# Kernel optimization log

Hardware: AMD Instinct MI355X
Metric: run time of the kernel (lower is better)

## Reference

```python
import jax, jax.numpy as jnp
import numpy as np

DIM = 768
H = 12
HD = DIM // H  # 64
B = 16
N = 1025  # cls token + 1024 patches; RoPE applied to tokens 1:


def setup_inputs() -> dict:
    key = jax.random.key(0)
    k1, k2, k3, k4, k5, k6 = jax.random.split(key, 6)
    x = jax.random.normal(k1, (B, N, DIM), dtype=jnp.float32)
    # rotary angles for the N-1 non-cls tokens, HD//2 freq pairs
    theta = jax.random.uniform(k2, (N - 1, HD // 2), dtype=jnp.float32) * 2.0 * jnp.pi
    freqs_cos = jnp.cos(theta)
    freqs_sin = jnp.sin(theta)
    W_qkv = jax.random.normal(k3, (3 * DIM, DIM), dtype=jnp.float32) * 0.02
    W_proj = jax.random.normal(k4, (DIM, DIM), dtype=jnp.float32) * 0.02
    b_proj = jax.random.normal(k5, (DIM,), dtype=jnp.float32) * 0.02
    return {"x": x, "freqs_cos": freqs_cos, "freqs_sin": freqs_sin,
            "W_qkv": W_qkv, "W_proj": W_proj, "b_proj": b_proj}


def _apply_rope(t, cos, sin):
    # t: [b, h, m, d]; cos/sin: [m, d/2]. Pairs are interleaved (even, odd),
    # matching torch.view_as_complex on a (..., d/2, 2) reshape.
    tr = t[..., 0::2]
    ti = t[..., 1::2]
    cos = cos[None, None, :, :]
    sin = sin[None, None, :, :]
    out_r = tr * cos - ti * sin
    out_i = tr * sin + ti * cos
    # interleave back: (..., d/2, 2) -> (..., d)
    out = jnp.stack([out_r, out_i], axis=-1)
    return out.reshape(t.shape)


def reference(x, freqs_cos, freqs_sin, W_qkv, W_proj, b_proj):
    b, n, dim = x.shape
    h, hd = H, HD
    scale = hd ** -0.5

    qkv = jnp.einsum('bnd,ed->bne', x, W_qkv)            # [b, n, 3*dim]
    qkv = qkv.reshape(b, n, 3, h, hd)
    q = jnp.transpose(qkv[:, :, 0], (0, 2, 1, 3))         # [b, h, n, hd]
    k = jnp.transpose(qkv[:, :, 1], (0, 2, 1, 3))
    v = jnp.transpose(qkv[:, :, 2], (0, 2, 1, 3))

    # RoPE on all tokens except the cls token (index 0)
    q = jnp.concatenate([q[:, :, :1], _apply_rope(q[:, :, 1:], freqs_cos, freqs_sin)], axis=2)
    k = jnp.concatenate([k[:, :, :1], _apply_rope(k[:, :, 1:], freqs_cos, freqs_sin)], axis=2)

    dots = jnp.einsum('bhid,bhjd->bhij', q, k) * scale    # [b, h, n, n]
    attn = jax.nn.softmax(dots, axis=-1)
    out = jnp.einsum('bhij,bhjd->bhid', attn, v)          # [b, h, n, hd]
    out = jnp.transpose(out, (0, 2, 1, 3)).reshape(b, n, dim)
    out = jnp.einsum('bnd,ed->bne', out, W_proj) + b_proj
    return out
```

## Files before the change

### kernel.cpp

```cpp
#include <hip/hip_runtime.h>
#include <stdint.h>

#define NH 12
#define HD64 64
#define SEQ 1025
#define M_ROWS (16 * SEQ)
#define DIM 768
#define NPAD 1088

typedef __attribute__((ext_vector_type(8))) short bf16x8;
typedef __attribute__((ext_vector_type(4))) float f32x4;
typedef __attribute__((ext_vector_type(4))) short s16x4;

#define VMCNT(n) asm volatile("s_waitcnt vmcnt(" #n ")" ::: "memory")
#define LGKMCNT0 asm volatile("s_waitcnt lgkmcnt(0)" ::: "memory")

__device__ __forceinline__ short f2bf_rne(float f) {
    union { float f; uint32_t u; } c; c.f = f;
    uint32_t u = c.u + 0x7fffu + ((c.u >> 16) & 1u);
    return (short)(u >> 16);
}

__device__ __forceinline__ int cvt_pk_bf16(float lo, float hi) {
    int r;
    asm("v_cvt_pk_bf16_f32 %0, %1, %2" : "=v"(r) : "v"(lo), "v"(hi));
    return r;
}

__device__ __forceinline__ void gload_lds16(const void* g, void* l) {
    __builtin_amdgcn_global_load_lds(
        (const __attribute__((address_space(1))) void*)g,
        (__attribute__((address_space(3))) void*)l, 16, 0, 0);
}

__device__ __forceinline__ int xcd_chunk_swizzle(int orig, int nwg) {
    int q = nwg >> 3, r = nwg & 7;
    int xcd = orig & 7, i = orig >> 3;
    int start = (xcd < r) ? xcd * (q + 1) : r * (q + 1) + (xcd - r) * q;
    return start + i;
}

__global__ void f2bf_kernel(const float* __restrict__ in, short* __restrict__ out, int n4) {
    int i = blockIdx.x * blockDim.x + threadIdx.x;
    if (i < n4) {
        f32x4 f = ((const f32x4*)in)[i];
        s16x4 o;
        o[0] = f2bf_rne(f[0]); o[1] = f2bf_rne(f[1]);
        o[2] = f2bf_rne(f[2]); o[3] = f2bf_rne(f[3]);
        ((s16x4*)out)[i] = o;
    }
}

__global__ __launch_bounds__(256) void qkv_gemm_kernel(
    const short* __restrict__ xb, const short* __restrict__ wb,
    const float* __restrict__ fcos, const float* __restrict__ fsin,
    short* __restrict__ Qb, short* __restrict__ Kb, short* __restrict__ VTb)
{
    __shared__ short Alds[3][128 * 32];
    __shared__ short Blds[3][128 * 32];
    const int tid = threadIdx.x;
    const int lane = tid & 63, w = tid >> 6;
    const int wm = w >> 1, wn = w & 1;
    const int lr = lane & 15, lg = lane >> 4;
    const int tile = xcd_chunk_swizzle(blockIdx.x, 129 * 18);
    const int mt = tile / 18, nt = tile - (tile / 18) * 18;

    const int c0 = tid, c1 = 256 + tid;
    int ra0 = mt * 128 + (c0 >> 2); if (ra0 > M_ROWS - 1) ra0 = M_ROWS - 1;
    int ra1 = mt * 128 + (c1 >> 2); if (ra1 > M_ROWS - 1) ra1 = M_ROWS - 1;
    const short* gA0 = xb + (size_t)ra0 * DIM + (c0 & 3) * 8;
    const short* gA1 = xb + (size_t)ra1 * DIM + (c1 & 3) * 8;
    const short* gB0 = wb + (size_t)(nt * 128 + (c0 >> 2)) * DIM + (c0 & 3) * 8;
    const short* gB1 = wb + (size_t)(nt * 128 + (c1 >> 2)) * DIM + (c1 & 3) * 8;
    short* lA0 = &Alds[0][0] + c0 * 8;
    short* lA1 = &Alds[0][0] + c1 * 8;
    short* lB0 = &Blds[0][0] + c0 * 8;
    short* lB1 = &Blds[0][0] + c1 * 8;

    auto stage = [&](int buf, int kt) {
        const int ko = kt * 32;
        const int lo = buf * (128 * 32);
        gload_lds16(gA0 + ko, lA0 + lo);
        gload_lds16(gA1 + ko, lA1 + lo);
        gload_lds16(gB0 + ko, lB0 + lo);
        gload_lds16(gB1 + ko, lB1 + lo);
    };

    f32x4 acc[4][4];
#pragma unroll
    for (int i = 0; i < 4; i++)
#pragma unroll
        for (int j = 0; j < 4; j++) acc[i][j] = (f32x4)0.0f;

    stage(0, 0); stage(1, 1); stage(2, 2);

    int cur = 0;
    for (int t = 0; t < 24; ++t) {
        if (t <= 21) { VMCNT(8); } else if (t == 22) { VMCNT(4); } else { VMCNT(0); }
        __builtin_amdgcn_s_barrier();

        bf16x8 af[4], bfr[4];
        const short* Ab = &Alds[0][0] + cur * (128 * 32);
        const short* Bb = &Blds[0][0] + cur * (128 * 32);
#pragma unroll
        for (int mi = 0; mi < 4; mi++)
            af[mi] = *(const bf16x8*)&Ab[(wm * 64 + mi * 16 + lr) * 32 + lg * 8];
#pragma unroll
        for (int ni = 0; ni < 4; ni++)
            bfr[ni] = *(const bf16x8*)&Bb[(wn * 64 + ni * 16 + lr) * 32 + lg * 8];

        if (t <= 20) {
            LGKMCNT0;
            __builtin_amdgcn_s_barrier();
            stage(cur, t + 3);
        }

#pragma unroll
        for (int mi = 0; mi < 4; mi++)
#pragma unroll
            for (int ni = 0; ni < 4; ni++)
                acc[mi][ni] = __builtin_amdgcn_mfma_f32_16x16x32_bf16(af[mi], bfr[ni], acc[mi][ni], 0, 0, 0);

        cur = (cur == 2) ? 0 : cur + 1;
    }

#pragma unroll
    for (int mi = 0; mi < 4; mi++) {
        int mbase = mt * 128 + wm * 64 + mi * 16 + lg * 4;
#pragma unroll
        for (int j = 0; j < 4; j++) {
            int m = mbase + j;
            bool valid = (m < M_ROWS);
            int mm = valid ? m : 0;
            int b = mm / SEQ;
            int n = mm - b * SEQ;
#pragma unroll
            for (int ni = 0; ni < 4; ni++) {
                int e = nt * 128 + wn * 64 + ni * 16 + lr;
                int qkv = e / DIM;
                int rem = e - qkv * DIM;
                int h = rem >> 6, d = rem & 63;
                float v = acc[mi][ni][j];
                float vo = __shfl_xor(v, 1);
                float outv = v;
                if (qkv < 2 && n > 0) {
                    float cs = fcos[(n - 1) * 32 + (d >> 1)];
                    float sn = fsin[(n - 1) * 32 + (d >> 1)];
                    outv = (d & 1) ? (vo * sn + v * cs) : (v * cs - vo * sn);
                }
                if (qkv == 0) outv *= 0.180336881f;
                if (valid) {
                    short bv = f2bf_rne(outv);
                    size_t bh = (size_t)b * NH + h;
                    if (qkv == 0)      Qb[(bh * SEQ + n) * HD64 + d] = bv;
                    else if (qkv == 1) Kb[(bh * SEQ + n) * HD64 + d] = bv;
                    else               VTb[(bh * HD64 + d) * NPAD + n] = bv;
                }
            }
        }
    }
}

__global__ __launch_bounds__(256) void attn_kernel(
    const short* __restrict__ Qb, const short* __restrict__ Kb,
    const short* __restrict__ VTb, short* __restrict__ AO)
{
    __shared__ short Klds[2][64 * 64];
    __shared__ short Vlds[2][64 * 64];
    __shared__ int Plds[4][16 * 32];
    const int tid = threadIdx.x;
    const int lane = tid & 63, w = tid >> 6;
    const int lr = lane & 15, lg = lane >> 4;
    const int tile = xcd_chunk_swizzle(blockIdx.x, 17 * 192);
    const int bh = tile / 17, qt = tile - (tile / 17) * 17;
    const int b = bh / NH, h = bh - b * NH;

    const short* Qp = Qb + (size_t)bh * SEQ * HD64;
    const short* Kp = Kb + (size_t)bh * SEQ * HD64;
    const short* Vp = VTb + (size_t)bh * HD64 * NPAD;

    int qr = qt * 64 + w * 16 + lr; if (qr > SEQ - 1) qr = SEQ - 1;
    bf16x8 qf0 = *(const bf16x8*)&Qp[(size_t)qr * HD64 + 0 + lg * 8];
    bf16x8 qf1 = *(const bf16x8*)&Qp[(size_t)qr * HD64 + 32 + lg * 8];

    float m_i = -1e30f, l_i = 0.f;
    f32x4 acc[4];
#pragma unroll
    for (int vt = 0; vt < 4; vt++) acc[vt] = (f32x4)0.0f;

    int* pw = &Plds[w][0];
    const int pswz = (lr & 3) << 3;

    auto stageKV = [&](int buf, int t) {
        int k0 = t * 64;
#pragma unroll
        for (int i = 0; i < 2; i++) {
            int c = i * 256 + tid;
            int row = c >> 3, ccd = c & 7;
            int cl = ccd ^ (row & 7);
            int krow = k0 + row; if (krow > SEQ - 1) krow = SEQ - 1;
            gload_lds16(Kp + (size_t)krow * HD64 + cl * 8, &Klds[buf][c * 8]);
            gload_lds16(Vp + (size_t)row * NPAD + k0 + cl * 8, &Vlds[buf][c * 8]);
        }
    };

    stageKV(0, 0);
    asm volatile("s_waitcnt vmcnt(0)" ::: "memory");
    __syncthreads();

    for (int t = 0; t < 17; ++t) {
        int cur = t & 1;
        if (t < 16) stageKV(cur ^ 1, t + 1);

        f32x4 s[4];
#pragma unroll
        for (int k16 = 0; k16 < 4; k16++) {
            int krow = k16 * 16 + lr;
            bf16x8 kf0 = *(const bf16x8*)&Klds[cur][krow * 64 + ((0 + lg) ^ (krow & 7)) * 8];
            bf16x8 kf1 = *(const bf16x8*)&Klds[cur][krow * 64 + ((4 + lg) ^ (krow & 7)) * 8];
            f32x4 d = (f32x4)0.0f;
            d = __builtin_amdgcn_mfma_f32_16x16x32_bf16(kf0, qf0, d, 0, 0, 0);
            d = __builtin_amdgcn_mfma_f32_16x16x32_bf16(kf1, qf1, d, 0, 0, 0);
            s[k16] = d;
        }
        if (t == 16) {
            s[0][0] = (lg == 0) ? s[0][0] : -1e30f;
            s[0][1] = -1e30f; s[0][2] = -1e30f; s[0][3] = -1e30f;
#pragma unroll
            for (int k16 = 1; k16 < 4; k16++) { s[k16][0] = -1e30f; s[k16][1] = -1e30f; s[k16][2] = -1e30f; s[k16][3] = -1e30f; }
        }

        float a0 = fmaxf(s[0][0], s[0][1]), a1 = fmaxf(s[0][2], s[0][3]);
        float a2 = fmaxf(s[1][0], s[1][1]), a3 = fmaxf(s[1][2], s[1][3]);
        float a4 = fmaxf(s[2][0], s[2][1]), a5 = fmaxf(s[2][2], s[2][3]);
        float a6 = fmaxf(s[3][0], s[3][1]), a7 = fmaxf(s[3][2], s[3][3]);
        float b0 = fmaxf(fmaxf(a0, a1), fmaxf(a2, a3));
        float b1 = fmaxf(fmaxf(a4, a5), fmaxf(a6, a7));
        float pmax = fmaxf(b0, b1);
        pmax = fmaxf(pmax, __shfl_xor(pmax, 16));
        pmax = fmaxf(pmax, __shfl_xor(pmax, 32));

        if (__any(pmax > m_i + 11.54f)) {
            float mnew = fmaxf(m_i, pmax);
            float sc = exp2f(m_i - mnew);
            m_i = mnew;
            l_i *= sc;
#pragma unroll
            for (int j = 0; j < 4; j++) {
                float scj = __shfl(sc, 4 * lg + j);
#pragma unroll
                for (int vt = 0; vt < 4; vt++) acc[vt][j] *= scj;
            }
        }

#pragma unroll
        for (int k16 = 0; k16 < 4; k16++) {
#pragma unroll
            for (int j = 0; j < 4; j++) s[k16][j] = exp2f(s[k16][j] - m_i);
        }
        float r0 = (s[0][0] + s[0][1]) + (s[0][2] + s[0][3]);
        float r1 = (s[1][0] + s[1][1]) + (s[1][2] + s[1][3]);
        float r2 = (s[2][0] + s[2][1]) + (s[2][2] + s[2][3]);
        float r3 = (s[3][0] + s[3][1]) + (s[3][2] + s[3][3]);
        float rowsum = (r0 + r1) + (r2 + r3);
        rowsum += __shfl_xor(rowsum, 16);
        rowsum += __shfl_xor(rowsum, 32);
        l_i += rowsum;

#pragma unroll
        for (int k16 = 0; k16 < 4; k16++) {
            int pk0 = cvt_pk_bf16(s[k16][0], s[k16][1]);
            int pk1 = cvt_pk_bf16(s[k16][2], s[k16][3]);
            int pbase = 8 * k16 + 2 * lg;
            pw[lr * 32 + ((pbase + 0) ^ pswz)] = pk0;
            pw[lr * 32 + ((pbase + 1) ^ pswz)] = pk1;
        }
        bf16x8 pa0 = *(const bf16x8*)&pw[lr * 32 + ((4 * lg) ^ pswz)];
        bf16x8 pa1 = *(const bf16x8*)&pw[lr * 32 + ((16 + 4 * lg) ^ pswz)];

#pragma unroll
        for (int vt = 0; vt < 4; vt++) {
            int dr = vt * 16 + lr;
            bf16x8 vf0 = *(const bf16x8*)&Vlds[cur][dr * 64 + ((0 + lg) ^ (dr & 7)) * 8];
            bf16x8 vf1 = *(const bf16x8*)&Vlds[cur][dr * 64 + ((4 + lg) ^ (dr & 7)) * 8];
            acc[vt] = __builtin_amdgcn_mfma_f32_16x16x32_bf16(pa0, vf0, acc[vt], 0, 0, 0);
            acc[vt] = __builtin_amdgcn_mfma_f32_16x16x32_bf16(pa1, vf1, acc[vt], 0, 0, 0);
        }

        asm volatile("s_waitcnt vmcnt(0)" ::: "memory");
        __syncthreads();
    }

    float inv[4];
#pragma unroll
    for (int j = 0; j < 4; j++) inv[j] = 1.0f / __shfl(l_i, 4 * lg + j);
#pragma unroll
    for (int vt = 0; vt < 4; vt++) {
#pragma unroll
        for (int j = 0; j < 4; j++) {
            int qrow = qt * 64 + w * 16 + lg * 4 + j;
            if (qrow < SEQ) {
                AO[((size_t)(b * SEQ + qrow)) * DIM + h * HD64 + vt * 16 + lr] =
                    f2bf_rne(acc[vt][j] * inv[j]);
            }
        }
    }
}

__global__ __launch_bounds__(256) void proj_gemm_kernel(
    const short* __restrict__ ab, const short* __restrict__ wb,
    const float* __restrict__ bias, float* __restrict__ out)
{
    __shared__ short Alds[3][128 * 32];
    __shared__ short Blds[3][128 * 32];
    const int tid = threadIdx.x;
    const int lane = tid & 63, w = tid >> 6;
    const int wm = w >> 1, wn = w & 1;
    const int lr = lane & 15, lg = lane >> 4;
    const int tile = xcd_chunk_swizzle(blockIdx.x, 129 * 6);
    const int mt = tile / 6, nt = tile - (tile / 6) * 6;

    const int c0 = tid, c1 = 256 + tid;
    int ra0 = mt * 128 + (c0 >> 2); if (ra0 > M_ROWS - 1) ra0 = M_ROWS - 1;
    int ra1 = mt * 128 + (c1 >> 2); if (ra1 > M_ROWS - 1) ra1 = M_ROWS - 1;
    const short* gA0 = ab + (size_t)ra0 * DIM + (c0 & 3) * 8;
    const short* gA1 = ab + (size_t)ra1 * DIM + (c1 & 3) * 8;
    const short* gB0 = wb + (size_t)(nt * 128 + (c0 >> 2)) * DIM + (c0 & 3) * 8;
    const short* gB1 = wb + (size_t)(nt * 128 + (c1 >> 2)) * DIM + (c1 & 3) * 8;
    short* lA0 = &Alds[0][0] + c0 * 8;
    short* lA1 = &Alds[0][0] + c1 * 8;
    short* lB0 = &Blds[0][0] + c0 * 8;
    short* lB1 = &Blds[0][0] + c1 * 8;

    auto stage = [&](int buf, int kt) {
        const int ko = kt * 32;
        const int lo = buf * (128 * 32);
        gload_lds16(gA0 + ko, lA0 + lo);
        gload_lds16(gA1 + ko, lA1 + lo);
        gload_lds16(gB0 + ko, lB0 + lo);
        gload_lds16(gB1 + ko, lB1 + lo);
    };

    f32x4 acc[4][4];
#pragma unroll
    for (int i = 0; i < 4; i++)
#pragma unroll
        for (int j = 0; j < 4; j++) acc[i][j] = (f32x4)0.0f;

    stage(0, 0); stage(1, 1); stage(2, 2);

    int cur = 0;
    for (int t = 0; t < 24; ++t) {
        if (t <= 21) { VMCNT(8); } else if (t == 22) { VMCNT(4); } else { VMCNT(0); }
        __builtin_amdgcn_s_barrier();

        bf16x8 af[4], bfr[4];
        const short* Ab = &Alds[0][0] + cur * (128 * 32);
        const short* Bb = &Blds[0][0] + cur * (128 * 32);
#pragma unroll
        for (int mi = 0; mi < 4; mi++)
            af[mi] = *(const bf16x8*)&Ab[(wm * 64 + mi * 16 + lr) * 32 + lg * 8];
#pragma unroll
        for (int ni = 0; ni < 4; ni++)
            bfr[ni] = *(const bf16x8*)&Bb[(wn * 64 + ni * 16 + lr) * 32 + lg * 8];

        if (t <= 20) {
            LGKMCNT0;
            __builtin_amdgcn_s_barrier();
            stage(cur, t + 3);
        }

#pragma unroll
        for (int mi = 0; mi < 4; mi++)
#pragma unroll
            for (int ni = 0; ni < 4; ni++)
                acc[mi][ni] = __builtin_amdgcn_mfma_f32_16x16x32_bf16(af[mi], bfr[ni], acc[mi][ni], 0, 0, 0);

        cur = (cur == 2) ? 0 : cur + 1;
    }

#pragma unroll
    for (int ni = 0; ni < 4; ni++) {
        int e = nt * 128 + wn * 64 + ni * 16 + lr;
        float bv = bias[e];
#pragma unroll
        for (int mi = 0; mi < 4; mi++) {
#pragma unroll
            for (int j = 0; j < 4; j++) {
                int m = mt * 128 + wm * 64 + mi * 16 + lg * 4 + j;
                if (m < M_ROWS) out[(size_t)m * DIM + e] = acc[mi][ni][j] + bv;
            }
        }
    }
}

extern "C" void kernel_launch(void* const* d_in, const int* in_sizes, int n_in,
                              void* d_out, int out_size, void* d_ws, size_t ws_size,
                              hipStream_t stream) {
    const float* x     = (const float*)d_in[0];
    const float* fcos  = (const float*)d_in[1];
    const float* fsin  = (const float*)d_in[2];
    const float* wqkv  = (const float*)d_in[3];
    const float* wproj = (const float*)d_in[4];
    const float* bproj = (const float*)d_in[5];
    float* out = (float*)d_out;

    char* ws = (char*)d_ws;
    size_t off = 0;
    auto salloc = [&](size_t bytes) { void* p = ws + off; off += (bytes + 255) & ~(size_t)255; return p; };
    short* xb     = (short*)salloc((size_t)M_ROWS * DIM * 2);
    short* wqkvb  = (short*)salloc((size_t)2304 * DIM * 2);
    short* wprojb = (short*)salloc((size_t)DIM * DIM * 2);
    short* Qb     = (short*)salloc((size_t)192 * SEQ * HD64 * 2);
    short* Kb     = (short*)salloc((size_t)192 * SEQ * HD64 * 2);
    short* VTb    = (short*)salloc((size_t)192 * HD64 * NPAD * 2);
    short* AO     = (short*)salloc((size_t)M_ROWS * DIM * 2);

    {
        int n4 = M_ROWS * DIM / 4;
        f2bf_kernel<<<(n4 + 255) / 256, 256, 0, stream>>>(x, xb, n4);
    }
    {
        int n4 = 2304 * DIM / 4;
        f2bf_kernel<<<(n4 + 255) / 256, 256, 0, stream>>>(wqkv, wqkvb, n4);
    }
    {
        int n4 = DIM * DIM / 4;
        f2bf_kernel<<<(n4 + 255) / 256, 256, 0, stream>>>(wproj, wprojb, n4);
    }

    qkv_gemm_kernel<<<129 * 18, 256, 0, stream>>>(xb, wqkvb, fcos, fsin, Qb, Kb, VTb);
    attn_kernel<<<17 * 192, 256, 0, stream>>>(Qb, Kb, VTb, AO);
    proj_gemm_kernel<<<129 * 6, 256, 0, stream>>>(AO, wprojb, bproj, out);
}
```

Baseline: 336.4 us.

## Widen QKV GEMM tile, swizzle LDS, fuse casts, add MFMA priority hints

The QKV GEMM N-tile is widened from 128 to 256, so each wave computes 4x8 MFMA tiles and the grid halves. Its A/B LDS layout gets an XOR swizzle to reduce bank conflicts on fragment reads. The three fp32-to-bf16 cast launches are merged into one kernel, and s_setprio hints are wrapped around the MFMA blocks in attention. The wider tile raises register and LDS use per block (launch_bounds 256,2), which may limit occupancy.

```diff
diff --git a/kernel.cpp b/kernel.cpp
--- a/kernel.cpp
+++ b/kernel.cpp
@@ -40,74 +40,88 @@
     return start + i;
 }
 
-__global__ void f2bf_kernel(const float* __restrict__ in, short* __restrict__ out, int n4) {
+__global__ void f2bf3_kernel(const float* __restrict__ a, short* __restrict__ ao, int na4,
+                             const float* __restrict__ b, short* __restrict__ bo, int nb4,
+                             const float* __restrict__ c, short* __restrict__ co, int nc4) {
     int i = blockIdx.x * blockDim.x + threadIdx.x;
-    if (i < n4) {
-        f32x4 f = ((const f32x4*)in)[i];
-        s16x4 o;
-        o[0] = f2bf_rne(f[0]); o[1] = f2bf_rne(f[1]);
-        o[2] = f2bf_rne(f[2]); o[3] = f2bf_rne(f[3]);
-        ((s16x4*)out)[i] = o;
-    }
-}
-
-__global__ __launch_bounds__(256) void qkv_gemm_kernel(
+    const float* src; short* dst; int idx;
+    if (i < na4) { src = a; dst = ao; idx = i; }
+    else if (i < na4 + nb4) { src = b; dst = bo; idx = i - na4; }
+    else if (i < na4 + nb4 + nc4) { src = c; dst = co; idx = i - na4 - nb4; }
+    else return;
+    f32x4 f = ((const f32x4*)src)[idx];
+    s16x4 o;
+    o[0] = f2bf_rne(f[0]); o[1] = f2bf_rne(f[1]);
+    o[2] = f2bf_rne(f[2]); o[3] = f2bf_rne(f[3]);
+    ((s16x4*)dst)[idx] = o;
+}
+
+__global__ __launch_bounds__(256, 2) void qkv_gemm_kernel(
     const short* __restrict__ xb, const short* __restrict__ wb,
     const float* __restrict__ fcos, const float* __restrict__ fsin,
     short* __restrict__ Qb, short* __restrict__ Kb, short* __restrict__ VTb)
 {
     __shared__ short Alds[3][128 * 32];
-    __shared__ short Blds[3][128 * 32];
+    __shared__ short Blds[3][256 * 32];
     const int tid = threadIdx.x;
     const int lane = tid & 63, w = tid >> 6;
     const int wm = w >> 1, wn = w & 1;
     const int lr = lane & 15, lg = lane >> 4;
-    const int tile = xcd_chunk_swizzle(blockIdx.x, 129 * 18);
-    const int mt = tile / 18, nt = tile - (tile / 18) * 18;
-
-    const int c0 = tid, c1 = 256 + tid;
-    int ra0 = mt * 128 + (c0 >> 2); if (ra0 > M_ROWS - 1) ra0 = M_ROWS - 1;
-    int ra1 = mt * 128 + (c1 >> 2); if (ra1 > M_ROWS - 1) ra1 = M_ROWS - 1;
-    const short* gA0 = xb + (size_t)ra0 * DIM + (c0 & 3) * 8;
-    const short* gA1 = xb + (size_t)ra1 * DIM + (c1 & 3) * 8;
-    const short* gB0 = wb + (size_t)(nt * 128 + (c0 >> 2)) * DIM + (c0 & 3) * 8;
-    const short* gB1 = wb + (size_t)(nt * 128 + (c1 >> 2)) * DIM + (c1 & 3) * 8;
-    short* lA0 = &Alds[0][0] + c0 * 8;
-    short* lA1 = &Alds[0][0] + c1 * 8;
-    short* lB0 = &Blds[0][0] + c0 * 8;
-    short* lB1 = &Blds[0][0] + c1 * 8;
+    const int tile = xcd_chunk_swizzle(blockIdx.x, 129 * 9);
+    const int mt = tile / 9, nt = tile - (tile / 9) * 9;
+
+    const int ca0 = tid, ca1 = tid + 256;
+    int ra0 = mt * 128 + (ca0 >> 2); if (ra0 > M_ROWS - 1) ra0 = M_ROWS - 1;
+    int ra1 = mt * 128 + (ca1 >> 2); if (ra1 > M_ROWS - 1) ra1 = M_ROWS - 1;
+    const int ga0 = (ca0 & 3) ^ ((ca0 >> 2) & 3) ^ ((ca0 >> 4) & 1);
+    const int ga1 = (ca1 & 3) ^ ((ca1 >> 2) & 3) ^ ((ca1 >> 4) & 1);
+    const short* gA0 = xb + (size_t)ra0 * DIM + ga0 * 8;
+    const short* gA1 = xb + (size_t)ra1 * DIM + ga1 * 8;
+    short* lA0 = &Alds[0][0] + ca0 * 8;
+    short* lA1 = &Alds[0][0] + ca1 * 8;
+
+    const short* gB[4]; short* lB[4];
+#pragma unroll
+    for (int i = 0; i < 4; i++) {
+        int cb = tid + 256 * i;
+        int gb = (cb & 3) ^ ((cb >> 2) & 3) ^ ((cb >> 4) & 1);
+        gB[i] = wb + (size_t)(nt * 256 + (cb >> 2)) * DIM + gb * 8;
+        lB[i] = &Blds[0][0] + cb * 8;
+    }
 
     auto stage = [&](int buf, int kt) {
         const int ko = kt * 32;
-        const int lo = buf * (128 * 32);
-        gload_lds16(gA0 + ko, lA0 + lo);
-        gload_lds16(gA1 + ko, lA1 + lo);
-        gload_lds16(gB0 + ko, lB0 + lo);
-        gload_lds16(gB1 + ko, lB1 + lo);
+        gload_lds16(gA0 + ko, lA0 + buf * (128 * 32));
+        gload_lds16(gA1 + ko, lA1 + buf * (128 * 32));
+#pragma unroll
+        for (int i = 0; i < 4; i++)
+            gload_lds16(gB[i] + ko, lB[i] + buf * (256 * 32));
     };
 
-    f32x4 acc[4][4];
+    f32x4 acc[4][8];
 #pragma unroll
     for (int i = 0; i < 4; i++)
 #pragma unroll
-        for (int j = 0; j < 4; j++) acc[i][j] = (f32x4)0.0f;
+        for (int j = 0; j < 8; j++) acc[i][j] = (f32x4)0.0f;
 
     stage(0, 0); stage(1, 1); stage(2, 2);
+
+    const int ablk = (lg ^ (lr & 3) ^ ((lr >> 2) & 1)) * 8;
 
     int cur = 0;
     for (int t = 0; t < 24; ++t) {
-        if (t <= 21) { VMCNT(8); } else if (t == 22) { VMCNT(4); } else { VMCNT(0); }
+        if (t <= 21) { VMCNT(12); } else if (t == 22) { VMCNT(6); } else { VMCNT(0); }
         __builtin_amdgcn_s_barrier();
 
-        bf16x8 af[4], bfr[4];
+        bf16x8 af[4], bF[8];
         const short* Ab = &Alds[0][0] + cur * (128 * 32);
-        const short* Bb = &Blds[0][0] + cur * (128 * 32);
+        const short* Bb = &Blds[0][0] + cur * (256 * 32);
 #pragma unroll
         for (int mi = 0; mi < 4; mi++)
-            af[mi] = *(const bf16x8*)&Ab[(wm * 64 + mi * 16 + lr) * 32 + lg * 8];
-#pragma unroll
-        for (int ni = 0; ni < 4; ni++)
-            bfr[ni] = *(const bf16x8*)&Bb[(wn * 64 + ni * 16 + lr) * 32 + lg * 8];
+            af[mi] = *(const bf16x8*)&Ab[(wm * 64 + mi * 16 + lr) * 32 + ablk];
+#pragma unroll
+        for (int ni = 0; ni < 8; ni++)
+            bF[ni] = *(const bf16x8*)&Bb[(wn * 128 + ni * 16 + lr) * 32 + ablk];
 
         if (t <= 20) {
             LGKMCNT0;
@@ -118,8 +132,8 @@
 #pragma unroll
         for (int mi = 0; mi < 4; mi++)
 #pragma unroll
-            for (int ni = 0; ni < 4; ni++)
-                acc[mi][ni] = __builtin_amdgcn_mfma_f32_16x16x32_bf16(af[mi], bfr[ni], acc[mi][ni], 0, 0, 0);
+            for (int ni = 0; ni < 8; ni++)
+                acc[mi][ni] = __builtin_amdgcn_mfma_f32_16x16x32_bf16(af[mi], bF[ni], acc[mi][ni], 0, 0, 0);
 
         cur = (cur == 2) ? 0 : cur + 1;
     }
@@ -135,8 +149,8 @@
             int b = mm / SEQ;
             int n = mm - b * SEQ;
 #pragma unroll
-            for (int ni = 0; ni < 4; ni++) {
-                int e = nt * 128 + wn * 64 + ni * 16 + lr;
+            for (int ni = 0; ni < 8; ni++) {
+                int e = nt * 256 + wn * 128 + ni * 16 + lr;
                 int qkv = e / DIM;
                 int rem = e - qkv * DIM;
                 int h = rem >> 6, d = rem & 63;
@@ -213,6 +227,7 @@
         if (t < 16) stageKV(cur ^ 1, t + 1);
 
         f32x4 s[4];
+        __builtin_amdgcn_s_setprio(1);
 #pragma unroll
         for (int k16 = 0; k16 < 4; k16++) {
             int krow = k16 * 16 + lr;
@@ -223,6 +238,7 @@
             d = __builtin_amdgcn_mfma_f32_16x16x32_bf16(kf1, qf1, d, 0, 0, 0);
             s[k16] = d;
         }
+        __builtin_amdgcn_s_setprio(0);
         if (t == 16) {
             s[0][0] = (lg == 0) ? s[0][0] : -1e30f;
             s[0][1] = -1e30f; s[0][2] = -1e30f; s[0][3] = -1e30f;
@@ -278,6 +294,7 @@
         bf16x8 pa0 = *(const bf16x8*)&pw[lr * 32 + ((4 * lg) ^ pswz)];
         bf16x8 pa1 = *(const bf16x8*)&pw[lr * 32 + ((16 + 4 * lg) ^ pswz)];
 
+        __builtin_amdgcn_s_setprio(1);
 #pragma unroll
         for (int vt = 0; vt < 4; vt++) {
             int dr = vt * 16 + lr;
@@ -286,6 +303,7 @@
             acc[vt] = __builtin_amdgcn_mfma_f32_16x16x32_bf16(pa0, vf0, acc[vt], 0, 0, 0);
             acc[vt] = __builtin_amdgcn_mfma_f32_16x16x32_bf16(pa1, vf1, acc[vt], 0, 0, 0);
         }
+        __builtin_amdgcn_s_setprio(0);
 
         asm volatile("s_waitcnt vmcnt(0)" ::: "memory");
         __syncthreads();
@@ -417,19 +435,14 @@
     short* AO     = (short*)salloc((size_t)M_ROWS * DIM * 2);
 
     {
-        int n4 = M_ROWS * DIM / 4;
-        f2bf_kernel<<<(n4 + 255) / 256, 256, 0, stream>>>(x, xb, n4);
-    }
-    {
-        int n4 = 2304 * DIM / 4;
-        f2bf_kernel<<<(n4 + 255) / 256, 256, 0, stream>>>(wqkv, wqkvb, n4);
-    }
-    {
-        int n4 = DIM * DIM / 4;
-        f2bf_kernel<<<(n4 + 255) / 256, 256, 0, stream>>>(wproj, wprojb, n4);
-    }
-
-    qkv_gemm_kernel<<<129 * 18, 256, 0, stream>>>(xb, wqkvb, fcos, fsin, Qb, Kb, VTb);
+        int na4 = M_ROWS * DIM / 4;
+        int nb4 = 2304 * DIM / 4;
+        int nc4 = DIM * DIM / 4;
+        int tot = na4 + nb4 + nc4;
+        f2bf3_kernel<<<(tot + 255) / 256, 256, 0, stream>>>(x, xb, na4, wqkv, wqkvb, nb4, wproj, wprojb, nc4);
+    }
+
+    qkv_gemm_kernel<<<129 * 9, 256, 0, stream>>>(xb, wqkvb, fcos, fsin, Qb, Kb, VTb);
     attn_kernel<<<17 * 192, 256, 0, stream>>>(Qb, Kb, VTb, AO);
     proj_gemm_kernel<<<129 * 6, 256, 0, stream>>>(AO, wprojb, bproj, out);
 }
```

New measurement: 350.5 us. 4.2% more time.
